# Optimization experiments

Measured on AMD Instinct MI355X. Metric: run time of the kernel, lower is better.

The kernel has to match this reference:

```python
import jax, jax.numpy as jnp
import numpy as np

B, T, H, E2, NPIX, CDIM, VOCAB = 8, 8, 512, 512, 49, 2048, 10000


def setup_inputs() -> dict:
    key = jax.random.key(0)
    ks = jax.random.split(key, 24)

    def w(k, shape, scale=0.02):
        return jax.random.normal(k, shape, jnp.float32) * scale

    return {
        "x": jax.random.normal(ks[0], (B, T, E2), jnp.float32),
        "hiddens": jax.random.normal(ks[1], (B, T, H), jnp.float32),
        "cells": jax.random.normal(ks[2], (B, T, H), jnp.float32),
        "V": jax.random.normal(ks[3], (B, NPIX, CDIM), jnp.float32),
        # Sentinel params
        "Wsx": w(ks[4], (E2, H)), "Wsh": w(ks[5], (H, H)),
        # Atten params (stored as [in, out]; Linear(in, out, bias=False))
        "Wv": w(ks[6], (CDIM, NPIX)), "Wg": w(ks[7], (H, NPIX)),
        "Ws": w(ks[8], (H, NPIX)), "Wh": w(ks[9], (NPIX, 1)),
        "Wfeat": w(ks[10], (1, 512)), "Wcxt": w(ks[11], (512, 1)),
        "Wg2": w(ks[12], (H, 512)), "Wspat": w(ks[13], (CDIM, 512)),
        "Wchan": w(ks[14], (NPIX, 512)),
        "Wgvs": w(ks[15], (H, 512)), "Wgvc": w(ks[16], (H, 512)),
        "Wghs": w(ks[17], (H, 512)), "Wghc": w(ks[18], (H, 512)),
        # Final classifier (has bias)
        "Wmlp": w(ks[19], (H, VOCAB)), "bmlp": jnp.zeros((VOCAB,), jnp.float32),
    }


def _forward(x, hiddens, cells, V, Wsx, Wsh, Wv, Wg, Ws, Wh, Wfeat, Wcxt,
             Wg2, Wspat, Wchan, Wgvs, Wgvc, Wghs, Wghc, Wmlp, bmlp):
    b, t, hdim = hiddens.shape
    # shifted hidden states: [h0, h_0..h_{T-2}]
    h0 = jnp.zeros((b, 1, hdim), hiddens.dtype)
    h_prev = jnp.concatenate([h0, hiddens[:, :-1, :]], axis=1) if t > 1 else h0
    # Sentinel: s_t = sigmoid(Wx x + Wh h_{t-1}) * tanh(cell)
    s = jax.nn.sigmoid(x @ Wsx + h_prev @ Wsh) * jnp.tanh(cells)
    h = hiddens

    # ---- channel attention (alpha0) ----
    featmean = jnp.mean(V, axis=1)[..., None]          # [B, 2048, 1]
    feature_vec = featmean @ Wfeat                      # [B, 2048, 512]
    cxt_ = jnp.tanh(feature_vec[:, None, :, :] + (h @ Wg2)[:, :, None, :])  # [B,T,2048,512]
    cxt = (cxt_ @ Wcxt)[..., 0]                         # [B, T, 2048]
    alpha0 = jax.nn.softmax(cxt, axis=-1)               # channel weights

    # ---- spatial attention (alpha_t) over channel-reweighted features ----
    wf = alpha0[:, :, None, :] * V[:, None, :, :]       # [B, T, 49, 2048]
    content_v = jnp.tanh(wf @ Wv + (h @ Wg)[:, :, None, :])  # [B, T, 49, 49]
    z_t = (jnp.tanh(content_v) @ Wh)[..., 0]            # [B, T, 49]
    alpha_t = jax.nn.softmax(z_t, axis=-1)

    c_spatial = jnp.einsum('btk,bkd->btd', alpha_t, V)  # [B, T, 2048]
    c_channel = jnp.mean(wf, axis=-1)                   # [B, T, 49]
    spatial_info = c_spatial @ Wspat                    # [B, T, 512]
    channel_info = c_channel @ Wchan                    # [B, T, 512]

    # ---- sentinel gates ----
    s_gate = jax.nn.sigmoid(s @ Wgvs + h @ Wghs)
    c_gate = jax.nn.sigmoid(s @ Wgvc + h @ Wghc)

    # ---- beta (sentinel vs visual) ----
    content_s = s @ Ws + h @ Wg                         # [B, T, 49]
    z_ext = jnp.tanh(content_s) @ Wh                    # [B, T, 1]
    extended = jnp.concatenate([z_t, z_ext], axis=-1)   # [B, T, 50]
    alpha_hat = jax.nn.softmax(extended, axis=-1)
    beta = alpha_hat[:, :, -1:]                         # [B, T, 1]

    c_hat = s_gate * spatial_info + c_gate * channel_info
    scores = (c_hat + h) @ Wmlp + bmlp                  # [B, T, VOCAB]
    return scores, alpha_t, beta


def reference(x, hiddens, cells, V, Wsx, Wsh, Wv, Wg, Ws, Wh, Wfeat, Wcxt,
              Wg2, Wspat, Wchan, Wgvs, Wgvc, Wghs, Wghc, Wmlp, bmlp):
    return _forward(x, hiddens, cells, V, Wsx, Wsh, Wv, Wg, Ws, Wh, Wfeat, Wcxt,
                    Wg2, Wspat, Wchan, Wgvs, Wgvc, Wghs, Wghc, Wmlp, bmlp)
```

## Files before the change

kernel.cpp:

```cpp
#include <hip/hip_runtime.h>

#define H 512
#define NTOK 64
#define NPIX 49
#define CDIM 2048
#define VOCAB 10000

#define WS_S      0
#define WS_ST     32768
#define WS_HT     65536
#define WS_XT     98304
#define WS_HPT    131072
#define WS_FM     163840
#define WS_G2F    180224
#define WS_P1     212992
#define WS_P2     245760
#define WS_CCH    278528
#define WS_A0     331776
#define WS_CSPT   331776
#define WS_CHT    331776
#define WS_SG2S   462848
#define WS_GSPS   2035712
#define WS_MS     4132864
#define WS_SCS    6591488
#define WS_MF     9151488

#define OUT_ALPHA 640000
#define OUT_BETA  643136

typedef __attribute__((ext_vector_type(8))) short short8;
typedef __attribute__((ext_vector_type(4))) float floatx4;

__device__ __forceinline__ float rcp_fast(float x) {
#if __has_builtin(__builtin_amdgcn_rcpf)
  return __builtin_amdgcn_rcpf(x);
#else
  return 1.0f / x;
#endif
}
__device__ __forceinline__ float tanh_f(float x) {
  float e = __expf(2.0f * x);
  return 1.0f - 2.0f * rcp_fast(e + 1.0f);
}
__device__ __forceinline__ float sigmoid_f(float x) {
  return rcp_fast(1.0f + __expf(-x));
}
__device__ __forceinline__ short f2bf(float x) {
  union { float f; unsigned u; } un; un.f = x;
  unsigned r = un.u + 0x7FFFu + ((un.u >> 16) & 1u);
  return (short)(r >> 16);
}
__device__ __forceinline__ float bf2f(unsigned short h) {
  union { unsigned u; float f; } cv; cv.u = ((unsigned)h) << 16;
  return cv.f;
}

__global__ __launch_bounds__(256) void k_prep(const float* __restrict__ x,
    const float* __restrict__ hid, const float* __restrict__ V,
    float* __restrict__ ws) {
  int bid = blockIdx.x, tid = threadIdx.x;
  if (bid < 64) {
    int b = bid >> 3, c = (bid & 7) * 256 + tid;
    float s = 0.0f;
    for (int k = 0; k < NPIX; ++k) s += V[b * NPIX * CDIM + k * CDIM + c];
    ws[WS_FM + b * CDIM + c] = s * (1.0f / NPIX);
  } else {
    int i3 = (bid - 64) * 256 + tid;
    int role = i3 >> 15, idx = i3 & 32767;
    int n = idx >> 9, k = idx & 511;
    if (role == 0)      ws[WS_XT + k * 64 + n] = x[idx];
    else if (role == 1) ws[WS_HT + k * 64 + n] = hid[idx];
    else                ws[WS_HPT + k * 64 + n] = (n & 7) ? hid[idx - 512] : 0.0f;
  }
}

__device__ __forceinline__ void gemm16s(const float* __restrict__ A,
    const float* __restrict__ W, float* __restrict__ Cslab,
    int n0, int k0, int nk, int c) {
  float acc[16];
#pragma unroll
  for (int j = 0; j < 16; ++j) acc[j] = 0.0f;
#pragma unroll 4
  for (int kk = 0; kk < nk; ++kk) {
    int k = k0 + kk;
    float w = W[k * 512 + c];
    const float4* A4 = (const float4*)(A + k * 64 + n0);
#pragma unroll
    for (int q = 0; q < 4; ++q) {
      float4 a = A4[q];
      acc[q * 4 + 0] += a.x * w;
      acc[q * 4 + 1] += a.y * w;
      acc[q * 4 + 2] += a.z * w;
      acc[q * 4 + 3] += a.w * w;
    }
  }
#pragma unroll
  for (int j = 0; j < 16; ++j) Cslab[(n0 + j) * 512 + c] = acc[j];
}

__global__ __launch_bounds__(256) void k_gemm_sg2(const float* __restrict__ Wsx,
    const float* __restrict__ Wsh, const float* __restrict__ Wg2,
    float* __restrict__ ws) {
  int c = blockIdx.x * 256 + threadIdx.x;
  int kc = blockIdx.y;
  int z = blockIdx.z, st = z >> 2, n0 = (z & 3) * 16;
  const float* A = (st == 0) ? ws + WS_XT : (st == 1) ? ws + WS_HPT : ws + WS_HT;
  const float* W = (st == 0) ? Wsx : (st == 1) ? Wsh : Wg2;
  float* C = ws + WS_SG2S + (st * 16 + kc) * 32768;
  gemm16s(A, W, C, n0, kc * 32, 32, c);
}

__global__ __launch_bounds__(256) void k_act_s(const float* __restrict__ cells,
    float* __restrict__ ws) {
  int idx = blockIdx.x * 256 + threadIdx.x;
  int n = idx >> 9, c = idx & 511;
  float sa = 0.0f, g = 0.0f;
#pragma unroll
  for (int s = 0; s < 32; ++s) sa += ws[WS_SG2S + s * 32768 + idx];
#pragma unroll
  for (int s = 32; s < 48; ++s) g += ws[WS_SG2S + s * 32768 + idx];
  float v = sigmoid_f(sa) * tanh_f(cells[idx]);
  ws[WS_S + idx] = v;
  ws[WS_ST + c * 64 + n] = v;
  ws[WS_G2F + idx] = g;
}

__global__ __launch_bounds__(256) void k_mid(const float* __restrict__ Wfeat,
    const float* __restrict__ Wcxt, const float* __restrict__ Wgvs,
    const float* __restrict__ Wghs, const float* __restrict__ Wgvc,
    const float* __restrict__ Wghc, const float* __restrict__ hid,
    const float* __restrict__ Wg, const float* __restrict__ Ws_,
    float* __restrict__ ws) {
  int bid = blockIdx.x, tid = threadIdx.x;
  if (bid < 512) {
    __shared__ float2 fw[512];
    __shared__ float g2l[512];
    int n = bid & 63, b = n >> 3;
    int c = (bid >> 6) * 256 + tid;
    for (int i = tid; i < 512; i += 256) {
      fw[i] = make_float2(Wfeat[i], Wcxt[i]);
      g2l[i] = ws[WS_G2F + n * H + i];
    }
    __syncthreads();
    float fm = ws[WS_FM + b * CDIM + c];
    float acc = 0.0f;
#pragma unroll 4
    for (int j = 0; j < 512; ++j) {
      float2 p = fw[j];
      acc += tanh_f(fm * p.x + g2l[j]) * p.y;
    }
    ws[WS_A0 + n * CDIM + c] = acc;
  } else if (bid < 768) {
    int gi = bid - 512;
    int c = (gi & 1) * 256 + tid;
    int rest = gi >> 1;
    int kc = rest & 7;
    int zz = rest >> 3;
    int st = zz >> 2, n0 = (zz & 3) * 16;
    const float* A = ws + ((st & 1) ? WS_HT : WS_ST);
    const float* W = (st == 0) ? Wgvs : (st == 1) ? Wghs : (st == 2) ? Wgvc : Wghc;
    float* C = ws + WS_GSPS + (st * 8 + kc) * 32768;
    gemm16s(A, W, C, n0, kc * 64, 64, c);
  } else {
    int bidx = bid - 768;
    int n = bidx & 63, half = bidx >> 6;
    int k2 = tid & 63, w = tid >> 6;
    int kc = half * 4 + w;
    const float* hrow = hid + n * H;
    const float* srow = ws + WS_S + n * H;
    float a1 = 0.0f, a2 = 0.0f;
#pragma unroll 4
    for (int kk = 0; kk < 64; ++kk) {
      int k = kc * 64 + kk;
      if (k2 < NPIX) {
        a1 += hrow[k] * Wg[k * NPIX + k2];
        a2 += srow[k] * Ws_[k * NPIX + k2];
      }
    }
    if (k2 < NPIX) {
      ws[WS_P1 + (kc * 64 + n) * 64 + k2] = a1;
      ws[WS_P2 + (kc * 64 + n) * 64 + k2] = a2;
    }
  }
}

__global__ __launch_bounds__(256) void k_attnM(const float* __restrict__ V,
    const float* __restrict__ Wv, float* __restrict__ ws) {
  __shared__ __align__(16) short al[64 * 136];
  __shared__ __align__(16) short bl[64 * 136];
  __shared__ float red[8];
  int tid = threadIdx.x, bid = blockIdx.x;
  int kc = bid >> 6, n = bid & 63, b = n >> 3;
  int c0 = kc * 128;
  const float* cr = ws + WS_A0 + n * CDIM;
  const float* Vb = V + b * NPIX * CDIM + c0;
  int lane = tid & 63, w = tid >> 6;
  float v[8];
  float vmax = -1e30f;
#pragma unroll
  for (int i = 0; i < 8; ++i) { v[i] = cr[tid + i * 256]; vmax = fmaxf(vmax, v[i]); }
  for (int off = 32; off; off >>= 1) vmax = fmaxf(vmax, __shfl_xor(vmax, off));
  if (lane == 0) red[w] = vmax;
  __syncthreads();
  float m = fmaxf(fmaxf(red[0], red[1]), fmaxf(red[2], red[3]));
  float ss = 0.0f;
#pragma unroll
  for (int i = 0; i < 8; ++i) ss += __expf(v[i] - m);
  for (int off = 32; off; off >>= 1) ss += __shfl_xor(ss, off);
  if (lane == 0) red[4 + w] = ss;
  __syncthreads();
  float inv = rcp_fast(red[4] + red[5] + red[6] + red[7]);
  {
    int cc = tid & 127;
    float a0c = __expf(cr[c0 + cc] - m) * inv;
    for (int k = tid >> 7; k < NPIX; k += 2)
      al[k * 136 + cc] = f2bf(a0c * Vb[k * CDIM + cc]);
  }
  for (int idx = tid; idx < 128 * 64; idx += 256) {
    int cc = idx >> 6, r = idx & 63;
    if (r < NPIX) bl[r * 136 + cc] = f2bf(Wv[(c0 + cc) * NPIX + r]);
  }
  __syncthreads();
  if (tid < NPIX) {
    float cch = 0.0f;
    const unsigned short* ar = (const unsigned short*)(al + tid * 136);
#pragma unroll 8
    for (int cc = 0; cc < 128; ++cc) cch += bf2f(ar[cc]);
    ws[WS_CCH + (kc * 64 + n) * 52 + tid] = cch * (1.0f / CDIM);
  }
  int qm = lane >> 4, mr = lane & 15;
  floatx4 acc[4];
#pragma unroll
  for (int i = 0; i < 4; ++i) acc[i] = (floatx4){0.f, 0.f, 0.f, 0.f};
#pragma unroll
  for (int ks = 0; ks < 4; ++ks) {
    int cb = ks * 32 + qm * 8;
    short8 bf = *(const short8*)&bl[(w * 16 + mr) * 136 + cb];
#pragma unroll
    for (int i = 0; i < 4; ++i) {
      short8 af = *(const short8*)&al[(i * 16 + mr) * 136 + cb];
      acc[i] = __builtin_amdgcn_mfma_f32_16x16x32_bf16(af, bf, acc[i], 0, 0, 0);
    }
  }
  __syncthreads();
  float* ml = (float*)al;
  int k2 = w * 16 + mr;
  if (k2 < NPIX) {
#pragma unroll
    for (int i = 0; i < 4; ++i) {
#pragma unroll
      for (int r = 0; r < 4; ++r) {
        int kp = i * 16 + qm * 4 + r;
        if (kp < NPIX) ml[k2 * 49 + kp] = acc[i][r];
      }
    }
  }
  __syncthreads();
  float* Mp = ws + WS_MS + kc * 153664 + n * 2401;
  for (int idx = tid; idx < 2401; idx += 256) Mp[idx] = ml[idx];
}

__global__ __launch_bounds__(256) void k_redM(float* __restrict__ ws) {
  int n = blockIdx.y;
  int i = blockIdx.x * 256 + threadIdx.x;
  if (i < 2401) {
    float m = 0.0f;
#pragma unroll
    for (int s = 0; s < 16; ++s) m += ws[WS_MS + s * 153664 + n * 2401 + i];
    ws[WS_MF + n * 2401 + i] = m;
  }
}

__global__ __launch_bounds__(256) void k_zt(const float* __restrict__ Wh,
    float* __restrict__ ws, float* __restrict__ out) {
  __shared__ float gl[NPIX], cl[NPIX], whl[64];
  __shared__ float zbuf[4][64];
  int n = blockIdx.x, tid = threadIdx.x;
  if (tid < NPIX) {
    float s1 = 0.0f, s2 = 0.0f;
#pragma unroll
    for (int kc = 0; kc < 8; ++kc) {
      s1 += ws[WS_P1 + (kc * 64 + n) * 64 + tid];
      s2 += ws[WS_P2 + (kc * 64 + n) * 64 + tid];
    }
    gl[tid] = s1;
    cl[tid] = s1 + s2;
    whl[tid] = Wh[tid];
  }
  __syncthreads();
  int k = tid & 63, g = tid >> 6;
  float zp = 0.0f;
  if (k < NPIX) {
    int k2e = (g == 3) ? NPIX : (g * 13 + 13);
    const float* Mz = ws + WS_MF + n * 2401;
    for (int k2 = g * 13; k2 < k2e; ++k2) {
      float m = Mz[k2 * 49 + k];
      zp += tanh_f(tanh_f(m + gl[k2])) * whl[k2];
    }
  }
  zbuf[g][k] = zp;
  __syncthreads();
  if (tid < 64) {
    int lane = tid;
    float z = zbuf[0][lane] + zbuf[1][lane] + zbuf[2][lane] + zbuf[3][lane];
    float zm = (lane < NPIX) ? z : -1e30f;
    float m1 = zm;
    for (int off = 32; off; off >>= 1) m1 = fmaxf(m1, __shfl_xor(m1, off));
    float e = (lane < NPIX) ? __expf(z - m1) : 0.0f;
    float S1 = e;
    for (int off = 32; off; off >>= 1) S1 += __shfl_xor(S1, off);
    if (lane < NPIX) out[OUT_ALPHA + n * NPIX + lane] = e * rcp_fast(S1);
    float vz = (lane < NPIX) ? tanh_f(cl[lane]) * whl[lane] : 0.0f;
    for (int off = 32; off; off >>= 1) vz += __shfl_xor(vz, off);
    if (lane == 0) {
      float ze = vz;
      float m2 = fmaxf(m1, ze);
      float S2 = S1 * __expf(m1 - m2) + __expf(ze - m2);
      out[OUT_BETA + n] = __expf(ze - m2) * rcp_fast(S2);
    }
  }
}

__global__ __launch_bounds__(256) void k_cspatial(const float* __restrict__ V,
    const float* __restrict__ out, float* __restrict__ ws) {
  __shared__ float al[NPIX];
  int bid = blockIdx.x, tid = threadIdx.x;
  int n = bid & 63, b = n >> 3;
  int d = (bid >> 6) * 256 + tid;
  if (tid < NPIX) al[tid] = out[OUT_ALPHA + n * NPIX + tid];
  __syncthreads();
  float s = 0.0f;
#pragma unroll 7
  for (int k = 0; k < NPIX; ++k) s += al[k] * V[b * NPIX * CDIM + k * CDIM + d];
  ws[WS_CSPT + d * 64 + n] = s;
}

__global__ __launch_bounds__(256) void k_gemm_spat(const float* __restrict__ Wspat,
    float* __restrict__ ws) {
  int c = blockIdx.x * 256 + threadIdx.x;
  int kc = blockIdx.y;
  int z = blockIdx.z;
  int st = 4 + (z >> 2), n0 = (z & 3) * 16;
  int q = st - 4;
  const float* A = ws + WS_CSPT + q * 32768;
  const float* W = Wspat + q * 262144;
  float* C = ws + WS_GSPS + (st * 8 + kc) * 32768;
  gemm16s(A, W, C, n0, kc * 64, 64, c);
}

__global__ __launch_bounds__(256) void k_chat(const float* __restrict__ hid,
    const float* __restrict__ Wchan, float* __restrict__ ws) {
  __shared__ float cl[NPIX];
  int tid = threadIdx.x, n = blockIdx.y;
  int c = blockIdx.x * 256 + tid;
  if (tid < NPIX) {
    float s = 0.0f;
#pragma unroll
    for (int kc = 0; kc < 16; ++kc) s += ws[WS_CCH + (kc * 64 + n) * 52 + tid];
    cl[tid] = s;
  }
  __syncthreads();
  float acc = 0.0f;
#pragma unroll 7
  for (int k = 0; k < NPIX; ++k) acc += cl[k] * Wchan[k * H + c];
  int idx = n * H + c;
  float ga1 = 0.0f, ga2 = 0.0f, spat = 0.0f;
#pragma unroll
  for (int s = 0; s < 16; ++s)  ga1 += ws[WS_GSPS + s * 32768 + idx];
#pragma unroll
  for (int s = 16; s < 32; ++s) ga2 += ws[WS_GSPS + s * 32768 + idx];
#pragma unroll
  for (int s = 32; s < 64; ++s) spat += ws[WS_GSPS + s * 32768 + idx];
  float chat = sigmoid_f(ga1) * spat + sigmoid_f(ga2) * acc + hid[idx];
  ws[WS_CHT + c * 64 + n] = chat;
}

__global__ __launch_bounds__(256) void k_gemm_scores(const float* __restrict__ Wmlp,
    float* __restrict__ ws) {
  int tid = threadIdx.x;
  int c0 = blockIdx.x * 512 + tid * 2;
  if (c0 >= VOCAB) return;
  int kc = blockIdx.y, k0 = kc * 128;
  int n0 = blockIdx.z * 16;
  const float* A = ws + WS_CHT;
  const float2* W2 = (const float2*)Wmlp;
  int cw = c0 >> 1;
  float2 acc[16];
#pragma unroll
  for (int j = 0; j < 16; ++j) acc[j] = make_float2(0.f, 0.f);
#pragma unroll 4
  for (int kk = 0; kk < 128; ++kk) {
    int k = k0 + kk;
    float2 w = W2[k * (VOCAB / 2) + cw];
    const float4* A4 = (const float4*)(A + k * 64 + n0);
#pragma unroll
    for (int q = 0; q < 4; ++q) {
      float4 a = A4[q];
      acc[q * 4 + 0].x += a.x * w.x; acc[q * 4 + 0].y += a.x * w.y;
      acc[q * 4 + 1].x += a.y * w.x; acc[q * 4 + 1].y += a.y * w.y;
      acc[q * 4 + 2].x += a.z * w.x; acc[q * 4 + 2].y += a.z * w.y;
      acc[q * 4 + 3].x += a.w * w.x; acc[q * 4 + 3].y += a.w * w.y;
    }
  }
  float* slab = ws + WS_SCS + kc * 640000;
#pragma unroll
  for (int j = 0; j < 16; ++j)
    ((float2*)(slab + (n0 + j) * VOCAB))[cw] = acc[j];
}

__global__ __launch_bounds__(256) void k_red_scores(const float* __restrict__ bmlp,
    float* __restrict__ ws, float* __restrict__ out) {
  int c4 = blockIdx.x * 256 + threadIdx.x, n = blockIdx.y;
  if (c4 >= VOCAB / 4) return;
  const float4* b4 = (const float4*)bmlp;
  float4 v = b4[c4];
#pragma unroll
  for (int s = 0; s < 4; ++s) {
    float4 p = ((const float4*)(ws + WS_SCS + s * 640000 + n * VOCAB))[c4];
    v.x += p.x; v.y += p.y; v.z += p.z; v.w += p.w;
  }
  ((float4*)(out + n * VOCAB))[c4] = v;
}

extern "C" void kernel_launch(void* const* d_in, const int* in_sizes, int n_in,
                              void* d_out, int out_size, void* d_ws, size_t ws_size,
                              hipStream_t stream) {
  const float* x     = (const float*)d_in[0];
  const float* hid   = (const float*)d_in[1];
  const float* cells = (const float*)d_in[2];
  const float* V     = (const float*)d_in[3];
  const float* Wsx   = (const float*)d_in[4];
  const float* Wsh   = (const float*)d_in[5];
  const float* Wv    = (const float*)d_in[6];
  const float* Wg    = (const float*)d_in[7];
  const float* Ws_   = (const float*)d_in[8];
  const float* Wh    = (const float*)d_in[9];
  const float* Wfeat = (const float*)d_in[10];
  const float* Wcxt  = (const float*)d_in[11];
  const float* Wg2   = (const float*)d_in[12];
  const float* Wspat = (const float*)d_in[13];
  const float* Wchan = (const float*)d_in[14];
  const float* Wgvs  = (const float*)d_in[15];
  const float* Wgvc  = (const float*)d_in[16];
  const float* Wghs  = (const float*)d_in[17];
  const float* Wghc  = (const float*)d_in[18];
  const float* Wmlp  = (const float*)d_in[19];
  const float* bmlp  = (const float*)d_in[20];
  float* ws  = (float*)d_ws;
  float* out = (float*)d_out;

  hipLaunchKernelGGL(k_prep, dim3(448), dim3(256), 0, stream, x, hid, V, ws);
  hipLaunchKernelGGL(k_gemm_sg2, dim3(2, 16, 12), dim3(256), 0, stream, Wsx, Wsh, Wg2, ws);
  hipLaunchKernelGGL(k_act_s, dim3(128), dim3(256), 0, stream, cells, ws);
  hipLaunchKernelGGL(k_mid, dim3(896), dim3(256), 0, stream, Wfeat, Wcxt, Wgvs, Wghs, Wgvc, Wghc, hid, Wg, Ws_, ws);
  hipLaunchKernelGGL(k_attnM, dim3(1024), dim3(256), 0, stream, V, Wv, ws);
  hipLaunchKernelGGL(k_redM, dim3(10, 64), dim3(256), 0, stream, ws);
  hipLaunchKernelGGL(k_zt, dim3(64), dim3(256), 0, stream, Wh, ws, out);
  hipLaunchKernelGGL(k_cspatial, dim3(512), dim3(256), 0, stream, V, out, ws);
  hipLaunchKernelGGL(k_gemm_spat, dim3(2, 8, 16), dim3(256), 0, stream, Wspat, ws);
  hipLaunchKernelGGL(k_chat, dim3(2, 64), dim3(256), 0, stream, hid, Wchan, ws);
  hipLaunchKernelGGL(k_gemm_scores, dim3(20, 4, 4), dim3(256), 0, stream, Wmlp, ws);
  hipLaunchKernelGGL(k_red_scores, dim3(10, 64), dim3(256), 0, stream, bmlp, ws, out);
}
```

Baseline: 236.3 us.

## Use bf16 MFMA for vocab GEMM and fuse transposes into sentinel GEMMs

The final vocabulary projection now runs on bf16 MFMA 16x16x32 instructions. Each block converts a 128x64 tile of Wmlp to bf16 in shared memory, and the c_hat activations are written as row-major bf16 instead of transposed fp32. The separate transpose/prep kernel is merged into the sentinel GEMM kernel, which stages transposed activation tiles in LDS, and the gate GEMMs in k_mid read s and h directly the same way. This removes one launch and the transposed workspace copies. The cost is lower precision in the scores, because activations and weights are rounded to bf16.

```diff
diff --git a/kernel.cpp b/kernel.cpp
--- a/kernel.cpp
+++ b/kernel.cpp
@@ -7,10 +7,6 @@
 #define VOCAB 10000
 
 #define WS_S      0
-#define WS_ST     32768
-#define WS_HT     65536
-#define WS_XT     98304
-#define WS_HPT    131072
 #define WS_FM     163840
 #define WS_G2F    180224
 #define WS_P1     212992
@@ -55,73 +51,65 @@
   return cv.f;
 }
 
-__global__ __launch_bounds__(256) void k_prep(const float* __restrict__ x,
-    const float* __restrict__ hid, const float* __restrict__ V,
-    float* __restrict__ ws) {
+__global__ __launch_bounds__(256) void k_sg2(const float* __restrict__ Wsx,
+    const float* __restrict__ Wsh, const float* __restrict__ Wg2,
+    const float* __restrict__ x, const float* __restrict__ hid,
+    const float* __restrict__ V, float* __restrict__ ws) {
   int bid = blockIdx.x, tid = threadIdx.x;
-  if (bid < 64) {
-    int b = bid >> 3, c = (bid & 7) * 256 + tid;
+  if (bid < 384) {
+    __shared__ float aT[32 * 20];
+    int c2 = bid & 1, kc = (bid >> 1) & 15, z = bid >> 5;
+    int st = z >> 2, n0 = (z & 3) * 16;
+    int c = c2 * 256 + tid;
+    int k0 = kc * 32;
+    const float* W = (st == 0) ? Wsx : (st == 1) ? Wsh : Wg2;
+    for (int i = tid; i < 512; i += 256) {
+      int nn = i >> 5, kk = i & 31;
+      int tok = n0 + nn;
+      float v;
+      if (st == 0)      v = x[tok * 512 + k0 + kk];
+      else if (st == 1) v = (tok & 7) ? hid[(tok - 1) * 512 + k0 + kk] : 0.0f;
+      else              v = hid[tok * 512 + k0 + kk];
+      aT[kk * 20 + nn] = v;
+    }
+    __syncthreads();
+    float acc[16];
+#pragma unroll
+    for (int j = 0; j < 16; ++j) acc[j] = 0.0f;
+#pragma unroll 4
+    for (int kk = 0; kk < 32; ++kk) {
+      float w = W[(k0 + kk) * 512 + c];
+      const float4* a4 = (const float4*)&aT[kk * 20];
+#pragma unroll
+      for (int q = 0; q < 4; ++q) {
+        float4 a = a4[q];
+        acc[q * 4 + 0] += a.x * w;
+        acc[q * 4 + 1] += a.y * w;
+        acc[q * 4 + 2] += a.z * w;
+        acc[q * 4 + 3] += a.w * w;
+      }
+    }
+    float* C = ws + WS_SG2S + (st * 16 + kc) * 32768;
+#pragma unroll
+    for (int j = 0; j < 16; ++j) C[(n0 + j) * 512 + c] = acc[j];
+  } else {
+    int fb = bid - 384;
+    int b = fb >> 3, c = (fb & 7) * 256 + tid;
     float s = 0.0f;
     for (int k = 0; k < NPIX; ++k) s += V[b * NPIX * CDIM + k * CDIM + c];
     ws[WS_FM + b * CDIM + c] = s * (1.0f / NPIX);
-  } else {
-    int i3 = (bid - 64) * 256 + tid;
-    int role = i3 >> 15, idx = i3 & 32767;
-    int n = idx >> 9, k = idx & 511;
-    if (role == 0)      ws[WS_XT + k * 64 + n] = x[idx];
-    else if (role == 1) ws[WS_HT + k * 64 + n] = hid[idx];
-    else                ws[WS_HPT + k * 64 + n] = (n & 7) ? hid[idx - 512] : 0.0f;
-  }
-}
-
-__device__ __forceinline__ void gemm16s(const float* __restrict__ A,
-    const float* __restrict__ W, float* __restrict__ Cslab,
-    int n0, int k0, int nk, int c) {
-  float acc[16];
-#pragma unroll
-  for (int j = 0; j < 16; ++j) acc[j] = 0.0f;
-#pragma unroll 4
-  for (int kk = 0; kk < nk; ++kk) {
-    int k = k0 + kk;
-    float w = W[k * 512 + c];
-    const float4* A4 = (const float4*)(A + k * 64 + n0);
-#pragma unroll
-    for (int q = 0; q < 4; ++q) {
-      float4 a = A4[q];
-      acc[q * 4 + 0] += a.x * w;
-      acc[q * 4 + 1] += a.y * w;
-      acc[q * 4 + 2] += a.z * w;
-      acc[q * 4 + 3] += a.w * w;
-    }
-  }
-#pragma unroll
-  for (int j = 0; j < 16; ++j) Cslab[(n0 + j) * 512 + c] = acc[j];
-}
-
-__global__ __launch_bounds__(256) void k_gemm_sg2(const float* __restrict__ Wsx,
-    const float* __restrict__ Wsh, const float* __restrict__ Wg2,
-    float* __restrict__ ws) {
-  int c = blockIdx.x * 256 + threadIdx.x;
-  int kc = blockIdx.y;
-  int z = blockIdx.z, st = z >> 2, n0 = (z & 3) * 16;
-  const float* A = (st == 0) ? ws + WS_XT : (st == 1) ? ws + WS_HPT : ws + WS_HT;
-  const float* W = (st == 0) ? Wsx : (st == 1) ? Wsh : Wg2;
-  float* C = ws + WS_SG2S + (st * 16 + kc) * 32768;
-  gemm16s(A, W, C, n0, kc * 32, 32, c);
+  }
 }
 
 __global__ __launch_bounds__(256) void k_act_s(const float* __restrict__ cells,
     float* __restrict__ ws) {
   int idx = blockIdx.x * 256 + threadIdx.x;
-  int n = idx >> 9, c = idx & 511;
   float sa = 0.0f, g = 0.0f;
 #pragma unroll
   for (int s = 0; s < 32; ++s) sa += ws[WS_SG2S + s * 32768 + idx];
 #pragma unroll
   for (int s = 32; s < 48; ++s) g += ws[WS_SG2S + s * 32768 + idx];
-  float v = sigmoid_f(sa) * tanh_f(cells[idx]);
-  ws[WS_S + idx] = v;
-  ws[WS_ST + c * 64 + n] = v;
+  ws[WS_S + idx] = sigmoid_f(sa) * tanh_f(cells[idx]);
   ws[WS_G2F + idx] = g;
 }
 
@@ -151,16 +139,40 @@
     }
     ws[WS_A0 + n * CDIM + c] = acc;
   } else if (bid < 768) {
+    __shared__ float aT[64 * 20];
     int gi = bid - 512;
     int c = (gi & 1) * 256 + tid;
     int rest = gi >> 1;
     int kc = rest & 7;
     int zz = rest >> 3;
     int st = zz >> 2, n0 = (zz & 3) * 16;
-    const float* A = ws + ((st & 1) ? WS_HT : WS_ST);
+    int k0 = kc * 64;
+    const float* Asrc = (st & 1) ? hid : (ws + WS_S);
     const float* W = (st == 0) ? Wgvs : (st == 1) ? Wghs : (st == 2) ? Wgvc : Wghc;
+    for (int i = tid; i < 1024; i += 256) {
+      int nn = i >> 6, kk = i & 63;
+      aT[kk * 20 + nn] = Asrc[(n0 + nn) * 512 + k0 + kk];
+    }
+    __syncthreads();
+    float acc[16];
+#pragma unroll
+    for (int j = 0; j < 16; ++j) acc[j] = 0.0f;
+#pragma unroll 4
+    for (int kk = 0; kk < 64; ++kk) {
+      float w = W[(k0 + kk) * 512 + c];
+      const float4* a4 = (const float4*)&aT[kk * 20];
+#pragma unroll
+      for (int q = 0; q < 4; ++q) {
+        float4 a = a4[q];
+        acc[q * 4 + 0] += a.x * w;
+        acc[q * 4 + 1] += a.y * w;
+        acc[q * 4 + 2] += a.z * w;
+        acc[q * 4 + 3] += a.w * w;
+      }
+    }
     float* C = ws + WS_GSPS + (st * 8 + kc) * 32768;
-    gemm16s(A, W, C, n0, kc * 64, 64, c);
+#pragma unroll
+    for (int j = 0; j < 16; ++j) C[(n0 + j) * 512 + c] = acc[j];
   } else {
     int bidx = bid - 768;
     int n = bidx & 63, half = bidx >> 6;
@@ -344,8 +356,27 @@
   int q = st - 4;
   const float* A = ws + WS_CSPT + q * 32768;
   const float* W = Wspat + q * 262144;
+  int k0 = kc * 64;
+  float acc[16];
+#pragma unroll
+  for (int j = 0; j < 16; ++j) acc[j] = 0.0f;
+#pragma unroll 4
+  for (int kk = 0; kk < 64; ++kk) {
+    int k = k0 + kk;
+    float w = W[k * 512 + c];
+    const float4* A4 = (const float4*)(A + k * 64 + n0);
+#pragma unroll
+    for (int q2 = 0; q2 < 4; ++q2) {
+      float4 a = A4[q2];
+      acc[q2 * 4 + 0] += a.x * w;
+      acc[q2 * 4 + 1] += a.y * w;
+      acc[q2 * 4 + 2] += a.z * w;
+      acc[q2 * 4 + 3] += a.w * w;
+    }
+  }
   float* C = ws + WS_GSPS + (st * 8 + kc) * 32768;
-  gemm16s(A, W, C, n0, kc * 64, 64, c);
+#pragma unroll
+  for (int j = 0; j < 16; ++j) C[(n0 + j) * 512 + c] = acc[j];
 }
 
 __global__ __launch_bounds__(256) void k_chat(const float* __restrict__ hid,
@@ -372,40 +403,49 @@
 #pragma unroll
   for (int s = 32; s < 64; ++s) spat += ws[WS_GSPS + s * 32768 + idx];
   float chat = sigmoid_f(ga1) * spat + sigmoid_f(ga2) * acc + hid[idx];
-  ws[WS_CHT + c * 64 + n] = chat;
+  ((short*)(ws + WS_CHT))[idx] = f2bf(chat);
 }
 
 __global__ __launch_bounds__(256) void k_gemm_scores(const float* __restrict__ Wmlp,
     float* __restrict__ ws) {
+  __shared__ __align__(16) short bl[64 * 136];
   int tid = threadIdx.x;
-  int c0 = blockIdx.x * 512 + tid * 2;
-  if (c0 >= VOCAB) return;
-  int kc = blockIdx.y, k0 = kc * 128;
-  int n0 = blockIdx.z * 16;
-  const float* A = ws + WS_CHT;
-  const float2* W2 = (const float2*)Wmlp;
-  int cw = c0 >> 1;
-  float2 acc[16];
-#pragma unroll
-  for (int j = 0; j < 16; ++j) acc[j] = make_float2(0.f, 0.f);
-#pragma unroll 4
-  for (int kk = 0; kk < 128; ++kk) {
-    int k = k0 + kk;
-    float2 w = W2[k * (VOCAB / 2) + cw];
-    const float4* A4 = (const float4*)(A + k * 64 + n0);
-#pragma unroll
-    for (int q = 0; q < 4; ++q) {
-      float4 a = A4[q];
-      acc[q * 4 + 0].x += a.x * w.x; acc[q * 4 + 0].y += a.x * w.y;
-      acc[q * 4 + 1].x += a.y * w.x; acc[q * 4 + 1].y += a.y * w.y;
-      acc[q * 4 + 2].x += a.z * w.x; acc[q * 4 + 2].y += a.z * w.y;
-      acc[q * 4 + 3].x += a.w * w.x; acc[q * 4 + 3].y += a.w * w.y;
+  int cb = blockIdx.x, kc = blockIdx.y;
+  int c0 = cb * 64, k0 = kc * 128;
+  const short* CHB = (const short*)(ws + WS_CHT);
+  int lane = tid & 63, w = tid >> 6;
+  int mr = lane & 15, kg = lane >> 4;
+  for (int i = tid; i < 128 * 64; i += 256) {
+    int kk = i >> 6, cc = i & 63;
+    int c = c0 + cc;
+    float v = (c < VOCAB) ? Wmlp[(k0 + kk) * VOCAB + c] : 0.0f;
+    bl[cc * 136 + kk] = f2bf(v);
+  }
+  __syncthreads();
+  floatx4 acc[4];
+#pragma unroll
+  for (int i = 0; i < 4; ++i) acc[i] = (floatx4){0.f, 0.f, 0.f, 0.f};
+#pragma unroll
+  for (int ks = 0; ks < 4; ++ks) {
+    short8 af = *(const short8*)&CHB[(w * 16 + mr) * 512 + k0 + ks * 32 + kg * 8];
+#pragma unroll
+    for (int ct = 0; ct < 4; ++ct) {
+      short8 bf = *(const short8*)&bl[(ct * 16 + mr) * 136 + ks * 32 + kg * 8];
+      acc[ct] = __builtin_amdgcn_mfma_f32_16x16x32_bf16(af, bf, acc[ct], 0, 0, 0);
     }
   }
   float* slab = ws + WS_SCS + kc * 640000;
 #pragma unroll
-  for (int j = 0; j < 16; ++j)
-    ((float2*)(slab + (n0 + j) * VOCAB))[cw] = acc[j];
+  for (int ct = 0; ct < 4; ++ct) {
+    int c = c0 + ct * 16 + mr;
+    if (c < VOCAB) {
+#pragma unroll
+      for (int r = 0; r < 4; ++r) {
+        int n = w * 16 + kg * 4 + r;
+        slab[n * VOCAB + c] = acc[ct][r];
+      }
+    }
+  }
 }
 
 __global__ __launch_bounds__(256) void k_red_scores(const float* __restrict__ bmlp,
@@ -449,8 +489,7 @@
   float* ws  = (float*)d_ws;
   float* out = (float*)d_out;
 
-  hipLaunchKernelGGL(k_prep, dim3(448), dim3(256), 0, stream, x, hid, V, ws);
-  hipLaunchKernelGGL(k_gemm_sg2, dim3(2, 16, 12), dim3(256), 0, stream, Wsx, Wsh, Wg2, ws);
+  hipLaunchKernelGGL(k_sg2, dim3(448), dim3(256), 0, stream, Wsx, Wsh, Wg2, x, hid, V, ws);
   hipLaunchKernelGGL(k_act_s, dim3(128), dim3(256), 0, stream, cells, ws);
   hipLaunchKernelGGL(k_mid, dim3(896), dim3(256), 0, stream, Wfeat, Wcxt, Wgvs, Wghs, Wgvc, Wghc, hid, Wg, Ws_, ws);
   hipLaunchKernelGGL(k_attnM, dim3(1024), dim3(256), 0, stream, V, Wv, ws);
@@ -459,6 +498,6 @@
   hipLaunchKernelGGL(k_cspatial, dim3(512), dim3(256), 0, stream, V, out, ws);
   hipLaunchKernelGGL(k_gemm_spat, dim3(2, 8, 16), dim3(256), 0, stream, Wspat, ws);
   hipLaunchKernelGGL(k_chat, dim3(2, 64), dim3(256), 0, stream, hid, Wchan, ws);
-  hipLaunchKernelGGL(k_gemm_scores, dim3(20, 4, 4), dim3(256), 0, stream, Wmlp, ws);
+  hipLaunchKernelGGL(k_gemm_scores, dim3(157, 4), dim3(256), 0, stream, Wmlp, ws);
   hipLaunchKernelGGL(k_red_scores, dim3(10, 64), dim3(256), 0, stream, bmlp, ws, out);
 }
```

New measurement: 221.2 us. 6.4% less time.
